# Kernel optimization log

Hardware: AMD Instinct MI355X
Metric: run time of the kernel (lower is better)

The kernel has to match this reference:

```python
import jax, jax.numpy as jnp
import numpy as np

D_MODEL = 1024
N_HEADS = 16
D_KEY = D_MODEL // N_HEADS


def setup_inputs() -> dict:
    key = jax.random.key(0)
    ks = jax.random.split(key, 11)
    s = 1.0 / np.sqrt(D_MODEL)
    inp = {
        'query': jax.random.normal(ks[0], (2, 2048, D_MODEL), dtype=jnp.float32),
        'key': jax.random.normal(ks[1], (2, 2048, D_MODEL), dtype=jnp.float32),
        'value': jax.random.normal(ks[2], (2, 2048, D_MODEL), dtype=jnp.float32),
        'Wq': jax.random.uniform(ks[3], (D_MODEL, D_MODEL), jnp.float32, -s, s),
        'bq': jax.random.uniform(ks[4], (D_MODEL,), jnp.float32, -s, s),
        'Wk': jax.random.uniform(ks[5], (D_MODEL, D_MODEL), jnp.float32, -s, s),
        'bk': jax.random.uniform(ks[6], (D_MODEL,), jnp.float32, -s, s),
        'Wv': jax.random.uniform(ks[7], (D_MODEL, D_MODEL), jnp.float32, -s, s),
        'bv': jax.random.uniform(ks[8], (D_MODEL,), jnp.float32, -s, s),
        'Wo': jax.random.uniform(ks[9], (D_MODEL, D_MODEL), jnp.float32, -s, s),
        'bo': jax.random.uniform(ks[10], (D_MODEL,), jnp.float32, -s, s),
    }
    return inp


def _split_heads(x):
    b, s, _ = x.shape
    return x.reshape(b, s, N_HEADS, D_KEY).transpose(0, 2, 1, 3)  # [b,h,s,dk]


def reference(query, key, value, Wq, bq, Wk, bk, Wv, bv, Wo, bo):
    q = _split_heads(query @ Wq.T + bq)
    k = _split_heads(key @ Wk.T + bk)
    v = _split_heads(value @ Wv.T + bv)
    scale = 1.0 / jnp.sqrt(jnp.float32(D_KEY))
    scores = jnp.einsum('bhqd,bhkd->bhqk', q, k) * scale  # [b,h,s,s]
    probs = jax.nn.softmax(scores, axis=-1)
    attn = jnp.einsum('bhqk,bhkd->bhqd', probs, v)
    b, h, s, dk = attn.shape
    combined = attn.transpose(0, 2, 1, 3).reshape(b, s, D_MODEL)
    return combined @ Wo.T + bo
```

## Files before the change

### kernel.cpp

```cpp
#include <hip/hip_runtime.h>
#include <hip/hip_bf16.h>

#define DEVI __device__ __forceinline__

typedef short bf16x8 __attribute__((ext_vector_type(8)));
typedef float f32x4  __attribute__((ext_vector_type(4)));

#define WS_XQ   0u
#define WS_XK   4194304u
#define WS_XV   8388608u
#define WS_WQ   12582912u
#define WS_WK   13631488u
#define WS_WV   14680064u
#define WS_WO   15728640u
#define WS_QB   16777216u
#define WS_KB   20971520u
#define WS_VT   25165824u
#define WS_CB   29360128u

#define QSCALE 0.18033688011112042f

DEVI short f2bf(float f) {
  union { float f; unsigned u; } c; c.f = f;
  return (short)((c.u + 0x8000u) >> 16);
}

DEVI unsigned pk2(float a, float b) {
  union { float f; unsigned u; } x, y; x.f = a; y.f = b;
  return ((x.u + 0x8000u) >> 16) | ((y.u + 0x8000u) & 0xffff0000u);
}

DEVI void async16(const short* g, const short* l) {
  __builtin_amdgcn_global_load_lds(
      (const __attribute__((address_space(1))) void*)g,
      (__attribute__((address_space(3))) void*)l, 16, 0, 0);
}

__global__ __launch_bounds__(256) void conv_kernel(
    const float* __restrict__ q, const float* __restrict__ k, const float* __restrict__ v,
    const float* __restrict__ Wq, const float* __restrict__ Wk,
    const float* __restrict__ Wv, const float* __restrict__ Wo,
    short* __restrict__ ws)
{
  size_t e = ((size_t)blockIdx.x * 256 + threadIdx.x) * 8;
  const float* src; short* dst; float sc = 1.0f;
  if (e < 12582912u) {
    size_t which = e >> 22;
    size_t off   = e & 4194303u;
    src = (which == 0 ? q : which == 1 ? k : v) + off;
    dst = ws + which * 4194304u + off;
  } else {
    size_t j = e - 12582912u;
    size_t which = j >> 20;
    size_t off   = j & 1048575u;
    src = (which == 0 ? Wq : which == 1 ? Wk : which == 2 ? Wv : Wo) + off;
    dst = ws + 12582912u + which * 1048576u + off;
    if (which == 0) sc = QSCALE;
  }
  float4 f0 = *(const float4*)src;
  float4 f1 = *(const float4*)(src + 4);
  int4 o;
  o.x = pk2(f0.x * sc, f0.y * sc);
  o.y = pk2(f0.z * sc, f0.w * sc);
  o.z = pk2(f1.x * sc, f1.y * sc);
  o.w = pk2(f1.z * sc, f1.w * sc);
  *(int4*)dst = o;
}

template <int BN>
DEVI void gemm_body(const short* __restrict__ A, const short* __restrict__ Bt,
                    const float* __restrict__ bias, void* __restrict__ C,
                    int outmode, float bscale)
{
  constexpr int Kd = 1024, Nd = 1024;
  constexpr int NT = BN / 32;
  __shared__ __attribute__((aligned(16))) short smem[2][4096 + BN * 32];

  const int tid  = threadIdx.x;
  const int lane = tid & 63;
  const int w    = tid >> 6;
  const int quad = lane >> 4, cl = lane & 15;
  const int m0 = blockIdx.y * 128, n0 = blockIdx.x * BN;
  const int wm = (w >> 1) * 64, wn = (w & 1) * (BN / 2);

  auto stage = [&](int k0, int buf) {
    short* Ab = &smem[buf][0];
    short* Bb = &smem[buf][4096];
#pragma unroll
    for (int i = 0; i < 2; ++i) {
      int f = (w * 2 + i) * 64 + lane;
      int r = f >> 2;
      int kb = (f & 3) ^ (r & 3) ^ ((r >> 2) & 1);
      async16(A + (size_t)(m0 + r) * Kd + k0 + kb * 8, Ab + f * 8);
    }
#pragma unroll
    for (int i = 0; i < BN / 64; ++i) {
      int f = (w * (BN / 64) + i) * 64 + lane;
      int r = f >> 2;
      int kb = (f & 3) ^ (r & 3) ^ ((r >> 2) & 1);
      async16(Bt + (size_t)(n0 + r) * Kd + k0 + kb * 8, Bb + f * 8);
    }
  };

  f32x4 acc[4][NT];
#pragma unroll
  for (int i = 0; i < 4; ++i)
#pragma unroll
    for (int j = 0; j < NT; ++j)
#pragma unroll
      for (int r = 0; r < 4; ++r) acc[i][j][r] = 0.0f;

  stage(0, 0);
  __builtin_amdgcn_s_waitcnt(0);
  __syncthreads();

  for (int j = 0; j < 32; ++j) {
    if (j < 31) stage((j + 1) * 32, (j + 1) & 1);
    const short* Ab = &smem[j & 1][0];
    const short* Bb = &smem[j & 1][4096];
    bf16x8 af[4], bfr[NT];
#pragma unroll
    for (int mt = 0; mt < 4; ++mt) {
      int r = wm + mt * 16 + cl;
      int off = r * 32 + ((quad ^ (r & 3) ^ ((r >> 2) & 1)) << 3);
      af[mt] = *(const bf16x8*)&Ab[off];
    }
#pragma unroll
    for (int nt = 0; nt < NT; ++nt) {
      int r = wn + nt * 16 + cl;
      int off = r * 32 + ((quad ^ (r & 3) ^ ((r >> 2) & 1)) << 3);
      bfr[nt] = *(const bf16x8*)&Bb[off];
    }
#pragma unroll
    for (int mt = 0; mt < 4; ++mt)
#pragma unroll
      for (int nt = 0; nt < NT; ++nt)
        acc[mt][nt] = __builtin_amdgcn_mfma_f32_16x16x32_bf16(af[mt], bfr[nt], acc[mt][nt], 0, 0, 0);
    __builtin_amdgcn_s_waitcnt(0);
    __syncthreads();
  }

  if (BN == 128 && outmode == 1) {
    short* flat = &smem[0][0];
#pragma unroll
    for (int mt = 0; mt < 4; ++mt)
#pragma unroll
      for (int nt = 0; nt < NT; ++nt) {
        int n_l = wn + nt * 16 + cl;
        float bv = bias[n0 + n_l] * bscale;
        int m_base = wm + mt * 16 + quad * 4;
        short4 pk;
        pk.x = f2bf(acc[mt][nt][0] + bv);
        pk.y = f2bf(acc[mt][nt][1] + bv);
        pk.z = f2bf(acc[mt][nt][2] + bv);
        pk.w = f2bf(acc[mt][nt][3] + bv);
        int u = m_base >> 2;
        int addr = n_l * 128 + ((u ^ (n_l & 31)) << 2);
        *(short4*)&flat[addr] = pk;
      }
    __syncthreads();
    short* Cs = (short*)C;
    int bb = m0 >> 11;
    int s0 = m0 & 2047;
#pragma unroll
    for (int p = 0; p < 4; ++p) {
      int n_l = w * 32 + p * 8 + (lane >> 3);
      int mb = (lane & 7) * 16;
      short4 t0, t1, t2, t3;
      {
        int u = (mb >> 2) + 0; t0 = *(short4*)&flat[n_l * 128 + ((u ^ (n_l & 31)) << 2)];
        u = (mb >> 2) + 1;     t1 = *(short4*)&flat[n_l * 128 + ((u ^ (n_l & 31)) << 2)];
        u = (mb >> 2) + 2;     t2 = *(short4*)&flat[n_l * 128 + ((u ^ (n_l & 31)) << 2)];
        u = (mb >> 2) + 3;     t3 = *(short4*)&flat[n_l * 128 + ((u ^ (n_l & 31)) << 2)];
      }
      size_t g = ((size_t)(bb * 1024 + n0 + n_l)) * 2048 + s0 + mb;
      *(short4*)&Cs[g]      = t0;
      *(short4*)&Cs[g + 4]  = t1;
      *(short4*)&Cs[g + 8]  = t2;
      *(short4*)&Cs[g + 12] = t3;
    }
    return;
  }

#pragma unroll
  for (int mt = 0; mt < 4; ++mt)
#pragma unroll
    for (int nt = 0; nt < NT; ++nt) {
      int n = n0 + wn + nt * 16 + cl;
      float bv = bias[n] * bscale;
#pragma unroll
      for (int r = 0; r < 4; ++r) {
        int m = m0 + wm + mt * 16 + quad * 4 + r;
        float val = acc[mt][nt][r] + bv;
        if (outmode == 2) ((float*)C)[(size_t)m * Nd + n] = val;
        else              ((short*)C)[(size_t)m * Nd + n] = f2bf(val);
      }
    }
}

__global__ __launch_bounds__(256, 3) void proj_gemm(
    short* ws, const float* __restrict__ bq, const float* __restrict__ bk,
    const float* __restrict__ bv)
{
  int z = blockIdx.z;
  const short* A; const short* W; const float* bias; void* C;
  int mode; float bscale = 1.0f;
  if (z == 0)      { A = ws + WS_XQ; W = ws + WS_WQ; bias = bq; C = ws + WS_QB; mode = 0; bscale = QSCALE; }
  else if (z == 1) { A = ws + WS_XK; W = ws + WS_WK; bias = bk; C = ws + WS_KB; mode = 0; }
  else             { A = ws + WS_XV; W = ws + WS_WV; bias = bv; C = ws + WS_VT; mode = 1; }
  gemm_body<128>(A, W, bias, C, mode, bscale);
}

__global__ __launch_bounds__(256, 3) void out_gemm(
    const short* __restrict__ ws, const float* __restrict__ bo, float* __restrict__ out)
{
  gemm_body<64>(ws + WS_CB, ws + WS_WO, bo, out, 2, 1.0f);
}

__global__ __launch_bounds__(256, 4) void flash_kernel(
    const short* __restrict__ Qb, const short* __restrict__ Kb,
    const short* __restrict__ Vt, short* __restrict__ comb)
{
  __shared__ __attribute__((aligned(16))) short QsPs[8192];
  __shared__ __attribute__((aligned(16))) short Ks[3][2048];
  __shared__ __attribute__((aligned(16))) short Vts[2][2048];

  const int tid = threadIdx.x, lane = tid & 63, w = tid >> 6;
  const int quad = lane >> 4, cl = lane & 15;
  const int b = blockIdx.z, h = blockIdx.y, q0 = blockIdx.x * 128;
  const int qrow_base = w * 32;

  const short* Qg = Qb + ((size_t)(b * 2048 + q0)) * 1024 + h * 64;
  const short* Kg = Kb + ((size_t)(b * 2048)) * 1024 + h * 64;
  const short* Vg = Vt + ((size_t)(b * 1024 + h * 64)) * 2048;

  auto stageK = [&](int j0, short* Kd) {
    int f = w * 64 + lane;
    int r = f >> 3;
    int kb = (f & 7) ^ (r & 7);
    async16(Kg + (size_t)(j0 + r) * 1024 + kb * 8, Kd + f * 8);
  };
  auto stageV = [&](int j0, short* Vd) {
    int f = w * 64 + lane;
    int r = f >> 2;
    int kb = (f & 3) ^ (r & 3) ^ ((r >> 2) & 1);
    async16(Vg + (size_t)r * 2048 + j0 + kb * 8, Vd + f * 8);
  };

#pragma unroll
  for (int i = 0; i < 4; ++i) {
    int f = (w * 4 + i) * 64 + lane;
    int r = f >> 3, kb = (f & 7) ^ (r & 7);
    async16(Qg + (size_t)r * 1024 + kb * 8, QsPs + f * 8);
  }
  stageK(0, Ks[0]);
  stageK(32, Ks[1]);
  stageV(0, Vts[0]);
  __builtin_amdgcn_s_waitcnt(0);

  bf16x8 qa[2][2];
#pragma unroll
  for (int qt = 0; qt < 2; ++qt)
#pragma unroll
    for (int ks = 0; ks < 2; ++ks) {
      int r = qrow_base + qt * 16 + cl;
      int off = r * 64 + ((((ks << 2) | quad) ^ (r & 7)) << 3);
      qa[qt][ks] = *(const bf16x8*)&QsPs[off];
    }
  __syncthreads();

  auto qk = [&](const short* Kc, f32x4 (&dst)[2][2]) {
#pragma unroll
    for (int m = 0; m < 2; ++m)
#pragma unroll
      for (int qt = 0; qt < 2; ++qt)
#pragma unroll
        for (int r = 0; r < 4; ++r) dst[m][qt][r] = 0.0f;
#pragma unroll
    for (int ks = 0; ks < 2; ++ks) {
      bf16x8 ka[2];
#pragma unroll
      for (int m = 0; m < 2; ++m) {
        int r = m * 16 + cl;
        int off = r * 64 + ((((ks << 2) | quad) ^ (r & 7)) << 3);
        ka[m] = *(const bf16x8*)&Kc[off];
      }
#pragma unroll
      for (int m = 0; m < 2; ++m)
#pragma unroll
        for (int qt = 0; qt < 2; ++qt)
          dst[m][qt] = __builtin_amdgcn_mfma_f32_16x16x32_bf16(ka[m], qa[qt][ks], dst[m][qt], 0, 0, 0);
    }
  };

  f32x4 sA[2][2], sB[2][2];
  f32x4 accO[2][4];
  f32x4 accL[2];
#pragma unroll
  for (int qt = 0; qt < 2; ++qt) {
#pragma unroll
    for (int r = 0; r < 4; ++r) accL[qt][r] = 0.0f;
#pragma unroll
    for (int d = 0; d < 4; ++d)
#pragma unroll
      for (int r = 0; r < 4; ++r) accO[qt][d][r] = 0.0f;
  }

  const bf16x8 ones = { 0x3F80, 0x3F80, 0x3F80, 0x3F80, 0x3F80, 0x3F80, 0x3F80, 0x3F80 };

  qk(Ks[0], sA);

  int r0 = 0, r1 = 1, r2 = 2;
  auto body = [&](int j, f32x4 (&cur)[2][2], f32x4 (&nxt)[2][2]) {
    if (j + 2 < 64) stageK((j + 2) * 32, Ks[r2]);
    if (j + 1 < 64) { stageV((j + 1) * 32, Vts[(j + 1) & 1]); qk(Ks[r1], nxt); }
#pragma unroll
    for (int m = 0; m < 2; ++m)
#pragma unroll
      for (int qt = 0; qt < 2; ++qt) {
        int qrow = qrow_base + qt * 16 + cl;
        int sw = (qrow & 3) ^ ((qrow >> 2) & 1);
        int u = m * 2 + (quad >> 1);
        int off = qrow * 32 + (((u ^ sw)) << 3) + ((quad & 1) << 2);
        int2 pk;
        pk.x = pk2(__builtin_amdgcn_exp2f(cur[m][qt][0]),
                   __builtin_amdgcn_exp2f(cur[m][qt][1]));
        pk.y = pk2(__builtin_amdgcn_exp2f(cur[m][qt][2]),
                   __builtin_amdgcn_exp2f(cur[m][qt][3]));
        *(int2*)&QsPs[off] = pk;
      }
    const short* Vc = Vts[j & 1];
    bf16x8 pa[2];
#pragma unroll
    for (int qt = 0; qt < 2; ++qt) {
      int qrow = qrow_base + qt * 16 + cl;
      int sw = (qrow & 3) ^ ((qrow >> 2) & 1);
      int off = qrow * 32 + ((quad ^ sw) << 3);
      pa[qt] = *(const bf16x8*)&QsPs[off];
      accL[qt] = __builtin_amdgcn_mfma_f32_16x16x32_bf16(pa[qt], ones, accL[qt], 0, 0, 0);
    }
#pragma unroll
    for (int d = 0; d < 4; ++d) {
      int rr = d * 16 + cl;
      int off = rr * 32 + ((quad ^ (rr & 3) ^ ((rr >> 2) & 1)) << 3);
      bf16x8 vb = *(const bf16x8*)&Vc[off];
#pragma unroll
      for (int qt = 0; qt < 2; ++qt)
        accO[qt][d] = __builtin_amdgcn_mfma_f32_16x16x32_bf16(pa[qt], vb, accO[qt][d], 0, 0, 0);
    }
    __builtin_amdgcn_s_waitcnt(0);
    __syncthreads();
    int t = r0; r0 = r1; r1 = r2; r2 = t;
  };

  for (int j = 0; j < 64; j += 2) {
    body(j, sA, sB);
    body(j + 1, sB, sA);
  }

#pragma unroll
  for (int qt = 0; qt < 2; ++qt) {
    float inv[4];
#pragma unroll
    for (int r = 0; r < 4; ++r) inv[r] = 1.0f / accL[qt][r];
#pragma unroll
    for (int d = 0; d < 4; ++d)
#pragma unroll
      for (int r = 0; r < 4; ++r) {
        int q = q0 + qrow_base + qt * 16 + quad * 4 + r;
        int dc = d * 16 + cl;
        comb[((size_t)(b * 2048 + q)) * 1024 + h * 64 + dc] = f2bf(accO[qt][d][r] * inv[r]);
      }
  }
}

extern "C" void kernel_launch(void* const* d_in, const int* in_sizes, int n_in,
                              void* d_out, int out_size, void* d_ws, size_t ws_size,
                              hipStream_t stream) {
  const float* q  = (const float*)d_in[0];
  const float* k  = (const float*)d_in[1];
  const float* v  = (const float*)d_in[2];
  const float* Wq = (const float*)d_in[3];
  const float* bq = (const float*)d_in[4];
  const float* Wk = (const float*)d_in[5];
  const float* bk = (const float*)d_in[6];
  const float* Wv = (const float*)d_in[7];
  const float* bv = (const float*)d_in[8];
  const float* Wo = (const float*)d_in[9];
  const float* bo = (const float*)d_in[10];
  short* ws = (short*)d_ws;
  float* out = (float*)d_out;

  conv_kernel<<<8192, 256, 0, stream>>>(q, k, v, Wq, Wk, Wv, Wo, ws);
  proj_gemm<<<dim3(8, 32, 3), 256, 0, stream>>>(ws, bq, bk, bv);
  flash_kernel<<<dim3(16, 16, 2), 256, 0, stream>>>(ws + WS_QB, ws + WS_KB, ws + WS_VT, ws + WS_CB);
  out_gemm<<<dim3(16, 32), 256, 0, stream>>>(ws, bo, out);
}
```

Before: 231.6 us.

## Restructure flash attention to 8 waves with 64-key tiles per iteration

Doubles the flash attention block to 512 threads. Each wave now owns 16 query rows instead of 32, and the key/value tile grows from 32 to 64 keys, which halves the loop trip count and the number of block barriers. The swizzles for staging V and for the P buffer are rewritten for 64-wide rows. In exchange, LDS use per block rises to about 56KB, which limits occupancy. Each K fragment loaded from LDS now feeds only one query tile, so LDS read traffic per MFMA goes up.

Measured after the change: 222.0 us. 4.1% less time.

```diff
diff --git a/kernel.cpp b/kernel.cpp
--- a/kernel.cpp
+++ b/kernel.cpp
@@ -217,18 +217,18 @@
   gemm_body<64>(ws + WS_CB, ws + WS_WO, bo, out, 2, 1.0f);
 }
 
-__global__ __launch_bounds__(256, 4) void flash_kernel(
+__global__ __launch_bounds__(512, 4) void flash_kernel(
     const short* __restrict__ Qb, const short* __restrict__ Kb,
     const short* __restrict__ Vt, short* __restrict__ comb)
 {
   __shared__ __attribute__((aligned(16))) short QsPs[8192];
-  __shared__ __attribute__((aligned(16))) short Ks[3][2048];
-  __shared__ __attribute__((aligned(16))) short Vts[2][2048];
+  __shared__ __attribute__((aligned(16))) short Ks[3][4096];
+  __shared__ __attribute__((aligned(16))) short Vts[2][4096];
 
   const int tid = threadIdx.x, lane = tid & 63, w = tid >> 6;
   const int quad = lane >> 4, cl = lane & 15;
   const int b = blockIdx.z, h = blockIdx.y, q0 = blockIdx.x * 128;
-  const int qrow_base = w * 32;
+  const int qrow_base = w * 16;
 
   const short* Qg = Qb + ((size_t)(b * 2048 + q0)) * 1024 + h * 64;
   const short* Kg = Kb + ((size_t)(b * 2048)) * 1024 + h * 64;
@@ -242,136 +242,117 @@
   };
   auto stageV = [&](int j0, short* Vd) {
     int f = w * 64 + lane;
-    int r = f >> 2;
-    int kb = (f & 3) ^ (r & 3) ^ ((r >> 2) & 1);
+    int r = f >> 3;
+    int kb = (f & 7) ^ (r & 7);
     async16(Vg + (size_t)r * 2048 + j0 + kb * 8, Vd + f * 8);
   };
 
 #pragma unroll
-  for (int i = 0; i < 4; ++i) {
-    int f = (w * 4 + i) * 64 + lane;
+  for (int i = 0; i < 2; ++i) {
+    int f = w * 128 + i * 64 + lane;
     int r = f >> 3, kb = (f & 7) ^ (r & 7);
     async16(Qg + (size_t)r * 1024 + kb * 8, QsPs + f * 8);
   }
   stageK(0, Ks[0]);
-  stageK(32, Ks[1]);
+  stageK(64, Ks[1]);
   stageV(0, Vts[0]);
   __builtin_amdgcn_s_waitcnt(0);
 
-  bf16x8 qa[2][2];
-#pragma unroll
-  for (int qt = 0; qt < 2; ++qt)
+  bf16x8 qa[2];
+#pragma unroll
+  for (int ks = 0; ks < 2; ++ks) {
+    int r = qrow_base + cl;
+    int off = r * 64 + ((((ks << 2) | quad) ^ (r & 7)) << 3);
+    qa[ks] = *(const bf16x8*)&QsPs[off];
+  }
+  __syncthreads();
+
+  auto qk = [&](const short* Kc, f32x4 (&dst)[4]) {
+#pragma unroll
+    for (int m = 0; m < 4; ++m)
+#pragma unroll
+      for (int r = 0; r < 4; ++r) dst[m][r] = 0.0f;
 #pragma unroll
     for (int ks = 0; ks < 2; ++ks) {
-      int r = qrow_base + qt * 16 + cl;
-      int off = r * 64 + ((((ks << 2) | quad) ^ (r & 7)) << 3);
-      qa[qt][ks] = *(const bf16x8*)&QsPs[off];
-    }
-  __syncthreads();
-
-  auto qk = [&](const short* Kc, f32x4 (&dst)[2][2]) {
-#pragma unroll
-    for (int m = 0; m < 2; ++m)
-#pragma unroll
-      for (int qt = 0; qt < 2; ++qt)
-#pragma unroll
-        for (int r = 0; r < 4; ++r) dst[m][qt][r] = 0.0f;
-#pragma unroll
-    for (int ks = 0; ks < 2; ++ks) {
-      bf16x8 ka[2];
-#pragma unroll
-      for (int m = 0; m < 2; ++m) {
+      bf16x8 ka[4];
+#pragma unroll
+      for (int m = 0; m < 4; ++m) {
         int r = m * 16 + cl;
         int off = r * 64 + ((((ks << 2) | quad) ^ (r & 7)) << 3);
         ka[m] = *(const bf16x8*)&Kc[off];
       }
 #pragma unroll
-      for (int m = 0; m < 2; ++m)
-#pragma unroll
-        for (int qt = 0; qt < 2; ++qt)
-          dst[m][qt] = __builtin_amdgcn_mfma_f32_16x16x32_bf16(ka[m], qa[qt][ks], dst[m][qt], 0, 0, 0);
-    }
-  };
-
-  f32x4 sA[2][2], sB[2][2];
-  f32x4 accO[2][4];
-  f32x4 accL[2];
-#pragma unroll
-  for (int qt = 0; qt < 2; ++qt) {
-#pragma unroll
-    for (int r = 0; r < 4; ++r) accL[qt][r] = 0.0f;
-#pragma unroll
-    for (int d = 0; d < 4; ++d)
-#pragma unroll
-      for (int r = 0; r < 4; ++r) accO[qt][d][r] = 0.0f;
-  }
+      for (int m = 0; m < 4; ++m)
+        dst[m] = __builtin_amdgcn_mfma_f32_16x16x32_bf16(ka[m], qa[ks], dst[m], 0, 0, 0);
+    }
+  };
+
+  f32x4 sA[4], sB[4];
+  f32x4 accO[4];
+  f32x4 accL;
+#pragma unroll
+  for (int r = 0; r < 4; ++r) accL[r] = 0.0f;
+#pragma unroll
+  for (int d = 0; d < 4; ++d)
+#pragma unroll
+    for (int r = 0; r < 4; ++r) accO[d][r] = 0.0f;
 
   const bf16x8 ones = { 0x3F80, 0x3F80, 0x3F80, 0x3F80, 0x3F80, 0x3F80, 0x3F80, 0x3F80 };
 
   qk(Ks[0], sA);
 
   int r0 = 0, r1 = 1, r2 = 2;
-  auto body = [&](int j, f32x4 (&cur)[2][2], f32x4 (&nxt)[2][2]) {
-    if (j + 2 < 64) stageK((j + 2) * 32, Ks[r2]);
-    if (j + 1 < 64) { stageV((j + 1) * 32, Vts[(j + 1) & 1]); qk(Ks[r1], nxt); }
-#pragma unroll
-    for (int m = 0; m < 2; ++m)
-#pragma unroll
-      for (int qt = 0; qt < 2; ++qt) {
-        int qrow = qrow_base + qt * 16 + cl;
-        int sw = (qrow & 3) ^ ((qrow >> 2) & 1);
-        int u = m * 2 + (quad >> 1);
-        int off = qrow * 32 + (((u ^ sw)) << 3) + ((quad & 1) << 2);
-        int2 pk;
-        pk.x = pk2(__builtin_amdgcn_exp2f(cur[m][qt][0]),
-                   __builtin_amdgcn_exp2f(cur[m][qt][1]));
-        pk.y = pk2(__builtin_amdgcn_exp2f(cur[m][qt][2]),
-                   __builtin_amdgcn_exp2f(cur[m][qt][3]));
-        *(int2*)&QsPs[off] = pk;
-      }
+  auto body = [&](int j, f32x4 (&cur)[4], f32x4 (&nxt)[4]) {
+    if (j + 2 < 32) stageK((j + 2) * 64, Ks[r2]);
+    if (j + 1 < 32) { stageV((j + 1) * 64, Vts[(j + 1) & 1]); qk(Ks[r1], nxt); }
+#pragma unroll
+    for (int m = 0; m < 4; ++m) {
+      int qrow = qrow_base + cl;
+      int u = m * 2 + (quad >> 1);
+      int off = qrow * 64 + ((u ^ (qrow & 7)) << 3) + ((quad & 1) << 2);
+      int2 pk;
+      pk.x = pk2(__builtin_amdgcn_exp2f(cur[m][0]),
+                 __builtin_amdgcn_exp2f(cur[m][1]));
+      pk.y = pk2(__builtin_amdgcn_exp2f(cur[m][2]),
+                 __builtin_amdgcn_exp2f(cur[m][3]));
+      *(int2*)&QsPs[off] = pk;
+    }
     const short* Vc = Vts[j & 1];
-    bf16x8 pa[2];
-#pragma unroll
-    for (int qt = 0; qt < 2; ++qt) {
-      int qrow = qrow_base + qt * 16 + cl;
-      int sw = (qrow & 3) ^ ((qrow >> 2) & 1);
-      int off = qrow * 32 + ((quad ^ sw) << 3);
-      pa[qt] = *(const bf16x8*)&QsPs[off];
-      accL[qt] = __builtin_amdgcn_mfma_f32_16x16x32_bf16(pa[qt], ones, accL[qt], 0, 0, 0);
-    }
-#pragma unroll
-    for (int d = 0; d < 4; ++d) {
-      int rr = d * 16 + cl;
-      int off = rr * 32 + ((quad ^ (rr & 3) ^ ((rr >> 2) & 1)) << 3);
-      bf16x8 vb = *(const bf16x8*)&Vc[off];
-#pragma unroll
-      for (int qt = 0; qt < 2; ++qt)
-        accO[qt][d] = __builtin_amdgcn_mfma_f32_16x16x32_bf16(pa[qt], vb, accO[qt][d], 0, 0, 0);
+#pragma unroll
+    for (int kt = 0; kt < 2; ++kt) {
+      int qrow = qrow_base + cl;
+      int off = qrow * 64 + ((((kt << 2) | quad) ^ (qrow & 7)) << 3);
+      bf16x8 pa = *(const bf16x8*)&QsPs[off];
+      accL = __builtin_amdgcn_mfma_f32_16x16x32_bf16(pa, ones, accL, 0, 0, 0);
+#pragma unroll
+      for (int d = 0; d < 4; ++d) {
+        int rr = d * 16 + cl;
+        int voff = rr * 64 + ((((kt << 2) | quad) ^ (rr & 7)) << 3);
+        bf16x8 vb = *(const bf16x8*)&Vc[voff];
+        accO[d] = __builtin_amdgcn_mfma_f32_16x16x32_bf16(pa, vb, accO[d], 0, 0, 0);
+      }
     }
     __builtin_amdgcn_s_waitcnt(0);
     __syncthreads();
     int t = r0; r0 = r1; r1 = r2; r2 = t;
   };
 
-  for (int j = 0; j < 64; j += 2) {
+  for (int j = 0; j < 32; j += 2) {
     body(j, sA, sB);
     body(j + 1, sB, sA);
   }
 
-#pragma unroll
-  for (int qt = 0; qt < 2; ++qt) {
-    float inv[4];
-#pragma unroll
-    for (int r = 0; r < 4; ++r) inv[r] = 1.0f / accL[qt][r];
-#pragma unroll
-    for (int d = 0; d < 4; ++d)
-#pragma unroll
-      for (int r = 0; r < 4; ++r) {
-        int q = q0 + qrow_base + qt * 16 + quad * 4 + r;
-        int dc = d * 16 + cl;
-        comb[((size_t)(b * 2048 + q)) * 1024 + h * 64 + dc] = f2bf(accO[qt][d][r] * inv[r]);
-      }
-  }
+  float inv[4];
+#pragma unroll
+  for (int r = 0; r < 4; ++r) inv[r] = 1.0f / accL[r];
+#pragma unroll
+  for (int d = 0; d < 4; ++d)
+#pragma unroll
+    for (int r = 0; r < 4; ++r) {
+      int q = q0 + qrow_base + quad * 4 + r;
+      int dc = d * 16 + cl;
+      comb[((size_t)(b * 2048 + q)) * 1024 + h * 64 + dc] = f2bf(accO[d][r] * inv[r]);
+    }
 }
 
 extern "C" void kernel_launch(void* const* d_in, const int* in_sizes, int n_in,
@@ -393,6 +374,6 @@
 
   conv_kernel<<<8192, 256, 0, stream>>>(q, k, v, Wq, Wk, Wv, Wo, ws);
   proj_gemm<<<dim3(8, 32, 3), 256, 0, stream>>>(ws, bq, bk, bv);
-  flash_kernel<<<dim3(16, 16, 2), 256, 0, stream>>>(ws + WS_QB, ws + WS_KB, ws + WS_VT, ws + WS_CB);
+  flash_kernel<<<dim3(16, 16, 2), 512, 0, stream>>>(ws + WS_QB, ws + WS_KB, ws + WS_VT, ws + WS_CB);
   out_gemm<<<dim3(16, 32), 256, 0, stream>>>(ws, bo, out);
 }
```
